# Performance work log

Hardware: AMD Instinct MI355X
Metric: run time of the kernel (lower is better)

## Reference

```python
import jax, jax.numpy as jnp
import numpy as np

B, INPUT_DIM, HEAD = 16384, 1024, 8
DIM = INPUT_DIM // HEAD


def setup_inputs() -> dict:
    key = jax.random.key(0)
    k1, k2, kw1, kb1, kw2, kw3 = jax.random.split(key, 6)
    x1 = jax.random.normal(k1, (B, INPUT_DIM), dtype=jnp.float32)
    x2 = jax.random.normal(k2, (B, INPUT_DIM), dtype=jnp.float32)
    s = 1.0 / np.sqrt(DIM)
    W1 = jax.random.uniform(kw1, (HEAD, DIM), jnp.float32, -s, s)   # per-head Linear(dim,1) weight
    b1 = jax.random.uniform(kb1, (HEAD,), jnp.float32, -s, s)       # per-head Linear(dim,1) bias
    W2 = jax.random.uniform(kw2, (HEAD, DIM), jnp.float32, -s, s)   # per-head Linear(dim,1,bias=False)
    W3 = jax.random.uniform(kw3, (HEAD, DIM, DIM), jnp.float32, -s, s)  # per-head Linear(dim,dim) [out,in]
    return {"x1": x1, "x2": x2, "W1": W1, "b1": b1, "W2": W2, "W3": W3}


def reference(x1, x2, W1, b1, W2, W3):
    b = x1.shape[0]
    h1 = x1.reshape(b, HEAD, DIM)
    h2 = x2.reshape(b, HEAD, DIM)
    # per-head scalar linears: [b, head]
    t1 = jnp.einsum('bhd,hd->bh', h1, W1) + b1
    t2 = jnp.einsum('bhd,hd->bh', h2, W2)
    # diag(w3(x1_h) @ x2_h^T) == sum((x1_h @ W3_h^T) * x2_h, -1), batched over heads
    proj = jnp.einsum('bhi,hoi->bho', h1, W3)
    t3 = jnp.sum(proj * h2, axis=-1)
    return jnp.sum(t1 + t2 + t3, axis=1)  # [b]
```

## Files before the change

### kernel.cpp

```cpp
#include <hip/hip_runtime.h>


#define NB 16384
#define NHEAD 8
#define NDIM 128

typedef __attribute__((ext_vector_type(8))) short bf16x8;
typedef __attribute__((ext_vector_type(4))) float f32x4;

__device__ __forceinline__ void gload_lds16(const void* g, void* l) {
    __builtin_amdgcn_global_load_lds(
        (const __attribute__((address_space(1))) unsigned*)g,
        (__attribute__((address_space(3))) unsigned*)l, 16, 0, 0);
}

__global__ __launch_bounds__(256) void prep_w3(
    const float* __restrict__ W3, short* __restrict__ whi,
    short* __restrict__ wlo)
{
    const int t    = blockIdx.x * 256 + threadIdx.x;
    const int lane = t & 63;
    const int nt   = (t >> 6) & 7;
    const int kk   = (t >> 9) & 3;
    const int h    = t >> 11;
    const int lm   = lane & 15;
    const int lg   = lane >> 4;

    const float* src = W3 + ((size_t)(h * NDIM + nt * 16 + lm)) * NDIM
                          + kk * 32 + lg * 8;
    const float4 a = *reinterpret_cast<const float4*>(src);
    const float4 b = *reinterpret_cast<const float4*>(src + 4);
    float xf[8] = {a.x, a.y, a.z, a.w, b.x, b.y, b.z, b.w};
    bf16x8 hi, lo;
#pragma unroll
    for (int j = 0; j < 8; ++j) {
        const unsigned u = __float_as_uint(xf[j]);
        hi[j] = (short)(u >> 16);
        const float hf = __uint_as_float(u & 0xffff0000u);
        lo[j] = (short)(__float_as_uint(xf[j] - hf) >> 16);
    }
    reinterpret_cast<bf16x8*>(whi)[t] = hi;
    reinterpret_cast<bf16x8*>(wlo)[t] = lo;
}

__global__ __launch_bounds__(256, 4) void bilinear_mfma(
    const float* __restrict__ x1, const float* __restrict__ x2,
    const float* __restrict__ W1, const float* __restrict__ W2,
    const short* __restrict__ whi, const short* __restrict__ wlo,
    float* __restrict__ psum)
{
    const int tid = threadIdx.x;
    const int w   = tid >> 6;
    const int l   = tid & 63;
    const int lm  = l & 15;
    const int lg  = l >> 4;
    const int bid = blockIdx.x;
    const int h   = bid & 7;
    const int b0  = (bid >> 3) * 64;
    const int bw  = b0 + w * 16;

    __shared__ short lhi[2][4096];
    __shared__ short llo[2][4096];

    const short* __restrict__ shi = whi + (size_t)h * 16384;
    const short* __restrict__ slo = wlo + (size_t)h * 16384;

    const float* __restrict__ w1base = W1 + h * NDIM;
    const float* __restrict__ x1base = x1 + (size_t)(bw + lm) * (NHEAD * NDIM)
                                          + h * NDIM + lg * 8;

    float x2r[4][8];
    {
        const float* x2base = x2 + (size_t)(bw + lg * 4) * (NHEAD * NDIM)
                                 + h * NDIM + lm;
#pragma unroll
        for (int r = 0; r < 4; ++r)
#pragma unroll
            for (int nt = 0; nt < 8; ++nt)
                x2r[r][nt] = x2base[(size_t)r * (NHEAD * NDIM) + nt * 16];
    }

    gload_lds16(shi + (size_t)(tid) * 8,        &lhi[0][(w * 64) * 8]);
    gload_lds16(shi + (size_t)(256 + tid) * 8,  &lhi[0][(256 + w * 64) * 8]);
    gload_lds16(slo + (size_t)(tid) * 8,        &llo[0][(w * 64) * 8]);
    gload_lds16(slo + (size_t)(256 + tid) * 8,  &llo[0][(256 + w * 64) * 8]);

    float4 pa = *reinterpret_cast<const float4*>(x1base);
    float4 pb = *reinterpret_cast<const float4*>(x1base + 4);

    f32x4 acc[8];
#pragma unroll
    for (int nt = 0; nt < 8; ++nt) acc[nt] = (f32x4)0.f;
    float t1 = 0.f;

    __syncthreads();

#pragma unroll
    for (int kk = 0; kk < 4; ++kk) {
        const int cur = kk & 1;
        const int nxt = cur ^ 1;

        if (kk < 3) {
            const size_t g0 = (size_t)((kk + 1) * 512 + tid) * 8;
            gload_lds16(shi + g0,            &lhi[nxt][(w * 64) * 8]);
            gload_lds16(shi + g0 + 256 * 8,  &lhi[nxt][(256 + w * 64) * 8]);
            gload_lds16(slo + g0,            &llo[nxt][(w * 64) * 8]);
            gload_lds16(slo + g0 + 256 * 8,  &llo[nxt][(256 + w * 64) * 8]);
        }
        const float4 ca = pa, cb = pb;
        if (kk < 3) {
            pa = *reinterpret_cast<const float4*>(x1base + (kk + 1) * 32);
            pb = *reinterpret_cast<const float4*>(x1base + (kk + 1) * 32 + 4);
        }

        bf16x8 ahi, alo;
        {
            const int k0 = kk * 32 + lg * 8;
            const float4 wa = *reinterpret_cast<const float4*>(w1base + k0);
            const float4 wb = *reinterpret_cast<const float4*>(w1base + k0 + 4);
            float xf[8]  = {ca.x, ca.y, ca.z, ca.w, cb.x, cb.y, cb.z, cb.w};
            float w1f[8] = {wa.x, wa.y, wa.z, wa.w, wb.x, wb.y, wb.z, wb.w};
#pragma unroll
            for (int j = 0; j < 8; ++j) {
                const unsigned u = __float_as_uint(xf[j]);
                ahi[j] = (short)(u >> 16);
                const float hf = __uint_as_float(u & 0xffff0000u);
                alo[j] = (short)(__float_as_uint(xf[j] - hf) >> 16);
                t1 += xf[j] * w1f[j];
            }
        }

#pragma unroll
        for (int nt = 0; nt < 8; ++nt) {
            const bf16x8 bhi = *reinterpret_cast<const bf16x8*>(
                &lhi[cur][nt * 512 + l * 8]);
            const bf16x8 blo = *reinterpret_cast<const bf16x8*>(
                &llo[cur][nt * 512 + l * 8]);
            acc[nt] = __builtin_amdgcn_mfma_f32_16x16x32_bf16(ahi, bhi, acc[nt], 0, 0, 0);
            acc[nt] = __builtin_amdgcn_mfma_f32_16x16x32_bf16(alo, bhi, acc[nt], 0, 0, 0);
            acc[nt] = __builtin_amdgcn_mfma_f32_16x16x32_bf16(ahi, blo, acc[nt], 0, 0, 0);
        }

        __syncthreads();
    }

    float w2v[8];
#pragma unroll
    for (int nt = 0; nt < 8; ++nt) w2v[nt] = W2[h * NDIM + nt * 16 + lm];

    float cr[4];
#pragma unroll
    for (int r = 0; r < 4; ++r) {
        float s = 0.f;
#pragma unroll
        for (int nt = 0; nt < 8; ++nt)
            s += (acc[nt][r] + w2v[nt]) * x2r[r][nt];
        cr[r] = s;
    }
#pragma unroll
    for (int m = 1; m < 16; m <<= 1)
#pragma unroll
        for (int r = 0; r < 4; ++r) cr[r] += __shfl_xor(cr[r], m, 64);

    float tf = t1;
    tf += __shfl_xor(tf, 16, 64);
    tf += __shfl_xor(tf, 32, 64);
#pragma unroll
    for (int r = 0; r < 4; ++r) cr[r] += __shfl(tf, lg * 4 + r, 64);

    if (lm == 0) {
        float4 st;
        st.x = cr[0]; st.y = cr[1]; st.z = cr[2]; st.w = cr[3];
        *reinterpret_cast<float4*>(&psum[(size_t)h * NB + bw + lg * 4]) = st;
    }
}

__global__ __launch_bounds__(256) void bilinear_reduce(
    const float* __restrict__ psum, const float* __restrict__ b1,
    float* __restrict__ out)
{
    const int i = blockIdx.x * 256 + threadIdx.x;
    float bs = 0.f;
#pragma unroll
    for (int hh = 0; hh < NHEAD; ++hh) bs += b1[hh];
    float s = bs;
#pragma unroll
    for (int hh = 0; hh < NHEAD; ++hh) s += psum[(size_t)hh * NB + i];
    out[i] = s;
}

extern "C" void kernel_launch(void* const* d_in, const int* in_sizes, int n_in,
                              void* d_out, int out_size, void* d_ws, size_t ws_size,
                              hipStream_t stream) {
    const float* x1 = (const float*)d_in[0];
    const float* x2 = (const float*)d_in[1];
    const float* W1 = (const float*)d_in[2];
    const float* b1 = (const float*)d_in[3];
    const float* W2 = (const float*)d_in[4];
    const float* W3 = (const float*)d_in[5];
    float* out = (float*)d_out;

    short* whi = (short*)d_ws;
    short* wlo = whi + (size_t)NHEAD * NDIM * NDIM;
    float* psum = (float*)((char*)d_ws + 512 * 1024);

    prep_w3<<<dim3(64), dim3(256), 0, stream>>>(W3, whi, wlo);
    bilinear_mfma<<<dim3(NB / 64 * NHEAD), dim3(256), 0, stream>>>(
        x1, x2, W1, W2, whi, wlo, psum);
    bilinear_reduce<<<dim3(NB / 256), dim3(256), 0, stream>>>(psum, b1, out);
}
```

Measured before the change: 38.21 us.

## Keep full per-head W3 split in LDS and loop blocks over four row tiles

Each block now loads the whole hi/lo bf16 W3 slice for its head into shared memory once, 64 KB per block. It then loops over four 64-row batch tiles, so the grid is a quarter the size and W3 is reused across tiles instead of being re-streamed for every 64 rows. The per-kk double-buffered loads and their barriers go away. In exchange, more LDS per block lowers occupancy (launch bounds drop to 2), and there are fewer blocks to hide latency of the x1/x2 streaming loads, which are not prefetched across tiles.

```diff
diff --git a/kernel.cpp b/kernel.cpp
--- a/kernel.cpp
+++ b/kernel.cpp
@@ -4,6 +4,7 @@
 #define NB 16384
 #define NHEAD 8
 #define NDIM 128
+#define MT 4
 
 typedef __attribute__((ext_vector_type(8))) short bf16x8;
 typedef __attribute__((ext_vector_type(4))) float f32x4;
@@ -43,11 +44,11 @@
     reinterpret_cast<bf16x8*>(wlo)[t] = lo;
 }
 
-__global__ __launch_bounds__(256, 4) void bilinear_mfma(
+__global__ __launch_bounds__(256, 2) void bilinear_mfma(
     const float* __restrict__ x1, const float* __restrict__ x2,
     const float* __restrict__ W1, const float* __restrict__ W2,
     const short* __restrict__ whi, const short* __restrict__ wlo,
-    float* __restrict__ psum)
+    float* __restrict__ psum, int mtCount)
 {
     const int tid = threadIdx.x;
     const int w   = tid >> 6;
@@ -56,122 +57,115 @@
     const int lg  = l >> 4;
     const int bid = blockIdx.x;
     const int h   = bid & 7;
-    const int b0  = (bid >> 3) * 64;
-    const int bw  = b0 + w * 16;
-
-    __shared__ short lhi[2][4096];
-    __shared__ short llo[2][4096];
+    const int bt0 = (bid >> 3) * (64 * MT);
+
+    __shared__ short lhi[4][4096];
+    __shared__ short llo[4][4096];
 
     const short* __restrict__ shi = whi + (size_t)h * 16384;
     const short* __restrict__ slo = wlo + (size_t)h * 16384;
-
     const float* __restrict__ w1base = W1 + h * NDIM;
-    const float* __restrict__ x1base = x1 + (size_t)(bw + lm) * (NHEAD * NDIM)
-                                          + h * NDIM + lg * 8;
-
-    float x2r[4][8];
-    {
-        const float* x2base = x2 + (size_t)(bw + lg * 4) * (NHEAD * NDIM)
-                                 + h * NDIM + lm;
-#pragma unroll
-        for (int r = 0; r < 4; ++r)
+
+#pragma unroll
+    for (int i = 0; i < 8; ++i) {
+        gload_lds16(shi + (size_t)(i * 256 + tid) * 8,
+                    &lhi[0][0] + (size_t)(i * 256 + w * 64) * 8);
+        gload_lds16(slo + (size_t)(i * 256 + tid) * 8,
+                    &llo[0][0] + (size_t)(i * 256 + w * 64) * 8);
+    }
+
+    float w2v[8];
+#pragma unroll
+    for (int nt = 0; nt < 8; ++nt) w2v[nt] = W2[h * NDIM + nt * 16 + lm];
+
+    __syncthreads();
+
+    for (int mt = 0; mt < mtCount; ++mt) {
+        const int bw = bt0 + mt * 64 + w * 16;
+
+        float x2r[4][8];
+        {
+            const float* x2base = x2 + (size_t)(bw + lg * 4) * (NHEAD * NDIM)
+                                     + h * NDIM + lm;
+#pragma unroll
+            for (int r = 0; r < 4; ++r)
+#pragma unroll
+                for (int nt = 0; nt < 8; ++nt)
+                    x2r[r][nt] = x2base[(size_t)r * (NHEAD * NDIM) + nt * 16];
+        }
+
+        const float* x1base = x1 + (size_t)(bw + lm) * (NHEAD * NDIM)
+                                 + h * NDIM + lg * 8;
+        float4 pa = *reinterpret_cast<const float4*>(x1base);
+        float4 pb = *reinterpret_cast<const float4*>(x1base + 4);
+
+        f32x4 acc[8];
+#pragma unroll
+        for (int nt = 0; nt < 8; ++nt) acc[nt] = (f32x4)0.f;
+        float t1 = 0.f;
+
+#pragma unroll
+        for (int kk = 0; kk < 4; ++kk) {
+            const float4 ca = pa, cb = pb;
+            if (kk < 3) {
+                pa = *reinterpret_cast<const float4*>(x1base + (kk + 1) * 32);
+                pb = *reinterpret_cast<const float4*>(x1base + (kk + 1) * 32 + 4);
+            }
+
+            bf16x8 ahi, alo;
+            {
+                const int k0 = kk * 32 + lg * 8;
+                const float4 wa = *reinterpret_cast<const float4*>(w1base + k0);
+                const float4 wb = *reinterpret_cast<const float4*>(w1base + k0 + 4);
+                float xf[8]  = {ca.x, ca.y, ca.z, ca.w, cb.x, cb.y, cb.z, cb.w};
+                float w1f[8] = {wa.x, wa.y, wa.z, wa.w, wb.x, wb.y, wb.z, wb.w};
+#pragma unroll
+                for (int j = 0; j < 8; ++j) {
+                    const unsigned u = __float_as_uint(xf[j]);
+                    ahi[j] = (short)(u >> 16);
+                    const float hf = __uint_as_float(u & 0xffff0000u);
+                    alo[j] = (short)(__float_as_uint(xf[j] - hf) >> 16);
+                    t1 += xf[j] * w1f[j];
+                }
+            }
+
+#pragma unroll
+            for (int nt = 0; nt < 8; ++nt) {
+                const bf16x8 bhi = *reinterpret_cast<const bf16x8*>(
+                    &lhi[kk][nt * 512 + l * 8]);
+                const bf16x8 blo = *reinterpret_cast<const bf16x8*>(
+                    &llo[kk][nt * 512 + l * 8]);
+                acc[nt] = __builtin_amdgcn_mfma_f32_16x16x32_bf16(ahi, bhi, acc[nt], 0, 0, 0);
+                acc[nt] = __builtin_amdgcn_mfma_f32_16x16x32_bf16(alo, bhi, acc[nt], 0, 0, 0);
+                acc[nt] = __builtin_amdgcn_mfma_f32_16x16x32_bf16(ahi, blo, acc[nt], 0, 0, 0);
+            }
+        }
+
+        float cr[4];
+#pragma unroll
+        for (int r = 0; r < 4; ++r) {
+            float s = 0.f;
 #pragma unroll
             for (int nt = 0; nt < 8; ++nt)
-                x2r[r][nt] = x2base[(size_t)r * (NHEAD * NDIM) + nt * 16];
-    }
-
-    gload_lds16(shi + (size_t)(tid) * 8,        &lhi[0][(w * 64) * 8]);
-    gload_lds16(shi + (size_t)(256 + tid) * 8,  &lhi[0][(256 + w * 64) * 8]);
-    gload_lds16(slo + (size_t)(tid) * 8,        &llo[0][(w * 64) * 8]);
-    gload_lds16(slo + (size_t)(256 + tid) * 8,  &llo[0][(256 + w * 64) * 8]);
-
-    float4 pa = *reinterpret_cast<const float4*>(x1base);
-    float4 pb = *reinterpret_cast<const float4*>(x1base + 4);
-
-    f32x4 acc[8];
-#pragma unroll
-    for (int nt = 0; nt < 8; ++nt) acc[nt] = (f32x4)0.f;
-    float t1 = 0.f;
-
-    __syncthreads();
-
-#pragma unroll
-    for (int kk = 0; kk < 4; ++kk) {
-        const int cur = kk & 1;
-        const int nxt = cur ^ 1;
-
-        if (kk < 3) {
-            const size_t g0 = (size_t)((kk + 1) * 512 + tid) * 8;
-            gload_lds16(shi + g0,            &lhi[nxt][(w * 64) * 8]);
-            gload_lds16(shi + g0 + 256 * 8,  &lhi[nxt][(256 + w * 64) * 8]);
-            gload_lds16(slo + g0,            &llo[nxt][(w * 64) * 8]);
-            gload_lds16(slo + g0 + 256 * 8,  &llo[nxt][(256 + w * 64) * 8]);
-        }
-        const float4 ca = pa, cb = pb;
-        if (kk < 3) {
-            pa = *reinterpret_cast<const float4*>(x1base + (kk + 1) * 32);
-            pb = *reinterpret_cast<const float4*>(x1base + (kk + 1) * 32 + 4);
-        }
-
-        bf16x8 ahi, alo;
-        {
-            const int k0 = kk * 32 + lg * 8;
-            const float4 wa = *reinterpret_cast<const float4*>(w1base + k0);
-            const float4 wb = *reinterpret_cast<const float4*>(w1base + k0 + 4);
-            float xf[8]  = {ca.x, ca.y, ca.z, ca.w, cb.x, cb.y, cb.z, cb.w};
-            float w1f[8] = {wa.x, wa.y, wa.z, wa.w, wb.x, wb.y, wb.z, wb.w};
-#pragma unroll
-            for (int j = 0; j < 8; ++j) {
-                const unsigned u = __float_as_uint(xf[j]);
-                ahi[j] = (short)(u >> 16);
-                const float hf = __uint_as_float(u & 0xffff0000u);
-                alo[j] = (short)(__float_as_uint(xf[j] - hf) >> 16);
-                t1 += xf[j] * w1f[j];
-            }
-        }
-
-#pragma unroll
-        for (int nt = 0; nt < 8; ++nt) {
-            const bf16x8 bhi = *reinterpret_cast<const bf16x8*>(
-                &lhi[cur][nt * 512 + l * 8]);
-            const bf16x8 blo = *reinterpret_cast<const bf16x8*>(
-                &llo[cur][nt * 512 + l * 8]);
-            acc[nt] = __builtin_amdgcn_mfma_f32_16x16x32_bf16(ahi, bhi, acc[nt], 0, 0, 0);
-            acc[nt] = __builtin_amdgcn_mfma_f32_16x16x32_bf16(alo, bhi, acc[nt], 0, 0, 0);
-            acc[nt] = __builtin_amdgcn_mfma_f32_16x16x32_bf16(ahi, blo, acc[nt], 0, 0, 0);
-        }
-
-        __syncthreads();
-    }
-
-    float w2v[8];
-#pragma unroll
-    for (int nt = 0; nt < 8; ++nt) w2v[nt] = W2[h * NDIM + nt * 16 + lm];
-
-    float cr[4];
-#pragma unroll
-    for (int r = 0; r < 4; ++r) {
-        float s = 0.f;
-#pragma unroll
-        for (int nt = 0; nt < 8; ++nt)
-            s += (acc[nt][r] + w2v[nt]) * x2r[r][nt];
-        cr[r] = s;
-    }
-#pragma unroll
-    for (int m = 1; m < 16; m <<= 1)
-#pragma unroll
-        for (int r = 0; r < 4; ++r) cr[r] += __shfl_xor(cr[r], m, 64);
-
-    float tf = t1;
-    tf += __shfl_xor(tf, 16, 64);
-    tf += __shfl_xor(tf, 32, 64);
-#pragma unroll
-    for (int r = 0; r < 4; ++r) cr[r] += __shfl(tf, lg * 4 + r, 64);
-
-    if (lm == 0) {
-        float4 st;
-        st.x = cr[0]; st.y = cr[1]; st.z = cr[2]; st.w = cr[3];
-        *reinterpret_cast<float4*>(&psum[(size_t)h * NB + bw + lg * 4]) = st;
+                s += (acc[nt][r] + w2v[nt]) * x2r[r][nt];
+            cr[r] = s;
+        }
+#pragma unroll
+        for (int m = 1; m < 16; m <<= 1)
+#pragma unroll
+            for (int r = 0; r < 4; ++r) cr[r] += __shfl_xor(cr[r], m, 64);
+
+        float tf = t1;
+        tf += __shfl_xor(tf, 16, 64);
+        tf += __shfl_xor(tf, 32, 64);
+#pragma unroll
+        for (int r = 0; r < 4; ++r) cr[r] += __shfl(tf, lg * 4 + r, 64);
+
+        if (lm == 0) {
+            float4 st;
+            st.x = cr[0]; st.y = cr[1]; st.z = cr[2]; st.w = cr[3];
+            *reinterpret_cast<float4*>(&psum[(size_t)h * NB + bw + lg * 4]) = st;
+        }
     }
 }
 
@@ -205,7 +199,7 @@
     float* psum = (float*)((char*)d_ws + 512 * 1024);
 
     prep_w3<<<dim3(64), dim3(256), 0, stream>>>(W3, whi, wlo);
-    bilinear_mfma<<<dim3(NB / 64 * NHEAD), dim3(256), 0, stream>>>(
-        x1, x2, W1, W2, whi, wlo, psum);
+    bilinear_mfma<<<dim3(NB / (64 * MT) * NHEAD), dim3(256), 0, stream>>>(
+        x1, x2, W1, W2, whi, wlo, psum, MT);
     bilinear_reduce<<<dim3(NB / 256), dim3(256), 0, stream>>>(psum, b1, out);
 }
```

Measured after the change: 96.49 us. 153% more time.
